# Kernel tuning notes

Hardware: AMD Instinct MI355X
Metric: run time of the kernel (lower is better)

The kernel has to match this reference:

```python
import jax, jax.numpy as jnp
import numpy as np

B, C, L = 4, 256, 4096
C8 = C // 8

def setup_inputs() -> dict:
    key = jax.random.key(0)
    ks = jax.random.split(key, 8)
    s = 1.0 / np.sqrt(C)
    x = jax.random.normal(ks[0], (B, C, L), dtype=jnp.float32)
    Wq = jax.random.normal(ks[1], (C8, C), dtype=jnp.float32) * s
    bq = jax.random.normal(ks[2], (C8,), dtype=jnp.float32) * s
    Wk = jax.random.normal(ks[3], (C8, C), dtype=jnp.float32) * s
    bk = jax.random.normal(ks[4], (C8,), dtype=jnp.float32) * s
    Wv = jax.random.normal(ks[5], (C, C), dtype=jnp.float32) * s
    bv = jax.random.normal(ks[6], (C,), dtype=jnp.float32) * s
    gamma = jax.random.normal(ks[7], (1,), dtype=jnp.float32) * 0.1
    return {"x": x, "Wq": Wq, "bq": bq, "Wk": Wk, "bk": bk, "Wv": Wv, "bv": bv, "gamma": gamma}

def reference(x, Wq, bq, Wk, bk, Wv, bv, gamma):
    # pointwise conv1d == channel matmul: [O,C] x [B,C,L] -> [B,O,L]
    q = jnp.einsum('oc,bcl->bol', Wq, x) + bq[None, :, None]   # [B, C8, L]
    k = jnp.einsum('oc,bcl->bol', Wk, x) + bk[None, :, None]   # [B, C8, L]
    v = jnp.einsum('oc,bcl->bol', Wv, x) + bv[None, :, None]   # [B, C,  L]
    # attention[b,i,j] = sum_c q[b,c,i] * k[b,c,j]
    attn = jnp.einsum('bci,bcj->bij', q, k)                    # [B, L, L]
    attn = jax.nn.softmax(attn, axis=-1)
    # out[b,c,i] = sum_j v[b,c,j] * attn[b,i,j]
    out = jnp.einsum('bcj,bij->bci', v, attn)                  # [B, C, L]
    return gamma * out + x
```

## Files before the change

### kernel.cpp

```cpp
#include <hip/hip_runtime.h>
#include <math.h>

#define BB 4
#define CC 256
#define LL 4096
#define DD 32
#define LOG2E 1.44269504088896f

typedef __attribute__((ext_vector_type(8))) short short8;
typedef __attribute__((ext_vector_type(4))) short short4v;
typedef __attribute__((ext_vector_type(4))) float f32x4;
typedef __attribute__((ext_vector_type(16))) float f32x16;
typedef __attribute__((ext_vector_type(4))) unsigned int uint4v;
typedef __attribute__((ext_vector_type(2))) unsigned int uint2v;

#define BARRIER() asm volatile("s_waitcnt lgkmcnt(0)\n\ts_barrier" ::: "memory")

__device__ inline unsigned short f2bf(float f) {
  union { float f; unsigned u; } v; v.f = f;
  unsigned r = v.u + 0x7fffu + ((v.u >> 16) & 1u);
  return (unsigned short)(r >> 16);
}

__device__ inline float fast_exp2(float x) {
#if __has_builtin(__builtin_amdgcn_exp2f)
  return __builtin_amdgcn_exp2f(x);
#else
  return exp2f(x);
#endif
}

__global__ __launch_bounds__(256) void wprep_kernel(
    const float* __restrict__ Wq, const float* __restrict__ Wk, const float* __restrict__ Wv,
    unsigned short* __restrict__ wf)
{
  const int t = threadIdx.x;
  const int ot = blockIdx.x >> 1;
  const int rep = blockIdx.x & 1;
  const int lane = t & 63, cl = lane & 15, q4 = lane >> 4;
  const int ks = (t >> 6) + 4 * rep;
  const int o = ot * 16 + cl;
  const int c = ks * 32 + q4 * 8;
  const float* src = (o < 32) ? (Wq + o * CC) : (o < 64) ? (Wk + (o - 32) * CC)
                                              : (Wv + (o - 64) * CC);
  const float sc = (o < 32) ? LOG2E : 1.0f;
  unsigned short p[8];
  #pragma unroll
  for (int j = 0; j < 8; ++j) p[j] = f2bf(src[c + j] * sc);
  uint4v u;
  u.x = (unsigned)p[0] | ((unsigned)p[1] << 16);
  u.y = (unsigned)p[2] | ((unsigned)p[3] << 16);
  u.z = (unsigned)p[4] | ((unsigned)p[5] << 16);
  u.w = (unsigned)p[6] | ((unsigned)p[7] << 16);
  *(uint4v*)(wf + ((size_t)(ot * 8 + ks) * 64 + lane) * 8) = u;
}

__global__ __launch_bounds__(512, 4) void qkv_kernel(
    const float* __restrict__ x, const unsigned short* __restrict__ wf,
    const float* __restrict__ bq, const float* __restrict__ bk, const float* __restrict__ bv,
    unsigned short* __restrict__ qF, unsigned short* __restrict__ kF,
    unsigned short* __restrict__ vF)
{
  __shared__ union {
    float xl[32 * 261];
    struct {
      unsigned short qk[32 * 72];
      __align__(16) unsigned short v[256 * 40];
    } ep;
  } sm;

  const int t = threadIdx.x;
  const int lane = t & 63, cl = lane & 15, q4 = lane >> 4;
  const int blk = blockIdx.x;
  const int b  = (blk & 7) >> 1;
  const int it = ((blk >> 3) << 1) + (blk & 1);
  const int i0 = it * 32;

  {
    const int ln8 = t & 7;
    #pragma unroll
    for (int p = 0; p < 4; ++p) {
      const int c = (t >> 3) + 64 * p;
      const f32x4 v = *(const f32x4*)(x + ((size_t)(b * CC + c)) * LL + i0 + ln8 * 4);
      #pragma unroll
      for (int k = 0; k < 4; ++k) sm.xl[(ln8 * 4 + k) * 261 + c] = v[k];
    }
  }
  __syncthreads();

  const int wi = (t >> 6) & 1, wo = t >> 7;
  const f32x4 zero = {0.f, 0.f, 0.f, 0.f};
  f32x4 acc[5];
  #pragma unroll
  for (int u = 0; u < 5; ++u) acc[u] = zero;

  for (int ks = 0; ks < 8; ++ks) {
    unsigned short p[8];
    #pragma unroll
    for (int j = 0; j < 8; ++j)
      p[j] = f2bf(sm.xl[(16 * wi + cl) * 261 + ks * 32 + q4 * 8 + j]);
    union { short8 s; uint4v u; } bfr;
    bfr.u.x = (unsigned)p[0] | ((unsigned)p[1] << 16);
    bfr.u.y = (unsigned)p[2] | ((unsigned)p[3] << 16);
    bfr.u.z = (unsigned)p[4] | ((unsigned)p[5] << 16);
    bfr.u.w = (unsigned)p[6] | ((unsigned)p[7] << 16);
    #pragma unroll
    for (int u = 0; u < 5; ++u) {
      const short8 a = *(const short8*)(wf + ((size_t)((wo * 5 + u) * 8 + ks) * 64 + lane) * 8);
      acc[u] = __builtin_amdgcn_mfma_f32_16x16x32_bf16(a, bfr.s, acc[u], 0, 0, 0);
    }
  }
  __syncthreads();

  #pragma unroll
  for (int u = 0; u < 5; ++u) {
    const int g = wo * 5 + u;
    if (g < 4) {
      short4v pk;
      #pragma unroll
      for (int r = 0; r < 4; ++r) {
        const int o = 16 * g + 4 * q4 + r;
        const float v = acc[u][r] + ((o < 32) ? bq[o] * LOG2E : bk[o - 32]);
        pk[r] = (short)f2bf(v);
      }
      *(short4v*)&sm.ep.qk[(16 * wi + cl) * 72 + 16 * g + 4 * q4] = pk;
    } else {
      #pragma unroll
      for (int r = 0; r < 4; ++r) {
        const int ch = 16 * (g - 4) + 4 * q4 + r;
        sm.ep.v[ch * 40 + 16 * wi + cl] = f2bf(acc[u][r] + bv[ch]);
      }
    }
  }
  __syncthreads();

  if (t < 256) {
    const int which = t >> 7;
    const int c = (t >> 6) & 1;
    const int l = t & 63, hi2 = l >> 5, ql2 = l & 31;
    const uint4v d = *(const uint4v*)&sm.ep.qk[ql2 * 72 + which * 32 + c * 16 + hi2 * 8];
    unsigned short* dstf = which ? kF : qF;
    *(uint4v*)(dstf + (((size_t)(b * 128 + it) * 2 + c) * 64 + l) * 8) = d;
  }
  #pragma unroll
  for (int rep = 0; rep < 2; ++rep) {
    const int slot = t + 512 * rep;
    const int fl = slot >> 6, l = slot & 63;
    const int g = fl >> 3, m = fl & 7;
    const int hi2 = l >> 5, cl2 = l & 31;
    const uint4v d = *(const uint4v*)&sm.ep.v[(32 * m + cl2) * 40 + g * 16 + hi2 * 8];
    *(uint4v*)(vF + (((size_t)(b * 256 + 2 * it + g) * 8 + m) * 64 + l) * 8) = d;
  }
}

__global__ __launch_bounds__(768, 3) void attn_kernel(
    const unsigned short* __restrict__ qF, const unsigned short* __restrict__ kF,
    const unsigned short* __restrict__ vF, const float* __restrict__ x,
    const float* __restrict__ gamma_p, float* __restrict__ out)
{
  __shared__ __align__(16) unsigned short P[2 * 8 * 2 * 2 * 512];
  __shared__ float l_lds[8][2][64];

  const int t = threadIdx.x;
  const int w = t >> 6, lane = t & 63, ql = lane & 31, hi = lane >> 5;
  const int blk = blockIdx.x;
  const int b  = (blk & 7) >> 1;
  const int it = ((blk >> 3) << 1) + (blk & 1);
  const int i0 = it * 64;

  if (w < 8) {
    const int pw = w;
    short8 qB[2][2];
    #pragma unroll
    for (int qt = 0; qt < 2; ++qt)
      #pragma unroll
      for (int c = 0; c < 2; ++c)
        qB[qt][c] = *(const short8*)(qF +
            (((size_t)(b * 128 + it * 2 + qt) * 2 + c) * 64 + lane) * 8);
    short8 kA[2];
    #pragma unroll
    for (int c = 0; c < 2; ++c)
      kA[c] = *(const short8*)(kF + (((size_t)(b * 128 + pw) * 2 + c) * 64 + lane) * 8);
    float l_r[2] = {0.f, 0.f};
    const f32x16 z16 = {0.f,0.f,0.f,0.f,0.f,0.f,0.f,0.f,0.f,0.f,0.f,0.f,0.f,0.f,0.f,0.f};

    auto produce = [&](int ss, int buf) {
      f32x16 S[2];
      __builtin_amdgcn_s_setprio(1);
      #pragma unroll
      for (int qt = 0; qt < 2; ++qt)
        S[qt] = __builtin_amdgcn_mfma_f32_32x32x16_bf16(kA[0], qB[qt][0], z16, 0, 0, 0);
      #pragma unroll
      for (int qt = 0; qt < 2; ++qt)
        S[qt] = __builtin_amdgcn_mfma_f32_32x32x16_bf16(kA[1], qB[qt][1], S[qt], 0, 0, 0);
      __builtin_amdgcn_s_setprio(0);
      const int ntile = ((ss + 1) & 15) * 8 + pw;
      #pragma unroll
      for (int c = 0; c < 2; ++c)
        kA[c] = *(const short8*)(kF + (((size_t)(b * 128 + ntile) * 2 + c) * 64 + lane) * 8);
      #pragma unroll
      for (int qt = 0; qt < 2; ++qt) {
        float ex[16];
        #pragma unroll
        for (int r = 0; r < 16; ++r) ex[r] = fast_exp2(S[qt][r]);
        l_r[qt] += ((((ex[0] + ex[1]) + (ex[2] + ex[3])) + ((ex[4] + ex[5]) + (ex[6] + ex[7])))
                 + (((ex[8] + ex[9]) + (ex[10] + ex[11])) + ((ex[12] + ex[13]) + (ex[14] + ex[15]))));
        #pragma unroll
        for (int c = 0; c < 2; ++c) {
          unsigned w0, w1, w2, w3;
          asm("v_cvt_pk_bf16_f32 %0, %1, %2" : "=v"(w0) : "v"(ex[8 * c + 0]), "v"(ex[8 * c + 1]));
          asm("v_cvt_pk_bf16_f32 %0, %1, %2" : "=v"(w1) : "v"(ex[8 * c + 2]), "v"(ex[8 * c + 3]));
          asm("v_cvt_pk_bf16_f32 %0, %1, %2" : "=v"(w2) : "v"(ex[8 * c + 4]), "v"(ex[8 * c + 5]));
          asm("v_cvt_pk_bf16_f32 %0, %1, %2" : "=v"(w3) : "v"(ex[8 * c + 6]), "v"(ex[8 * c + 7]));
          asm("v_permlane32_swap_b32 %0, %1" : "+v"(w0), "+v"(w2));
          asm("v_permlane32_swap_b32 %0, %1" : "+v"(w1), "+v"(w3));
          uint4v u; u.x = w0; u.y = w1; u.z = w2; u.w = w3;
          *(uint4v*)(&P[(((buf * 8 + pw) * 2 + qt) * 2 + c) * 512 + hi * 256 + ql * 8]) = u;
        }
      }
    };

    produce(0, 0);
    __syncthreads();
    for (int i = 0; i < 16; ++i) {
      if (i < 15) produce(i + 1, (i + 1) & 1);
      BARRIER();
    }
    l_lds[pw][0][lane] = l_r[0];
    l_lds[pw][1][lane] = l_r[1];
    BARRIER();
  } else {
    const int mq = w - 8;
    const unsigned short* vroot = vF + (size_t)b * (256 * 8 * 512) + lane * 8;
    f32x16 O[2][2];
    #pragma unroll
    for (int mi = 0; mi < 2; ++mi)
      #pragma unroll
      for (int qt = 0; qt < 2; ++qt) {
        const f32x16 z16 = {0.f,0.f,0.f,0.f,0.f,0.f,0.f,0.f,0.f,0.f,0.f,0.f,0.f,0.f,0.f,0.f};
        O[mi][qt] = z16;
      }
    short8 vA[4][2];
    #pragma unroll
    for (int s = 0; s < 4; ++s)
      #pragma unroll
      for (int mi = 0; mi < 2; ++mi)
        vA[s][mi] = *(const short8*)(vroot + ((size_t)(s * 8 + 2 * mq + mi)) * 512);
    __syncthreads();

    short8 pb[3][2];
    for (int i = 0; i < 16; ++i) {
      const int buf = i & 1;
      #pragma unroll
      for (int s = 0; s < 2; ++s)
        #pragma unroll
        for (int qt = 0; qt < 2; ++qt)
          pb[s][qt] = *(const short8*)(&P[((((buf * 8 + 0) * 2 + qt) * 2 + s) * 512)
                                          + hi * 256 + ql * 8]);
      #pragma unroll
      for (int s = 0; s < 16; ++s) {
        if (s < 14) {
          const int ns = s + 2, kk = ns >> 1, c = ns & 1;
          #pragma unroll
          for (int qt = 0; qt < 2; ++qt)
            pb[ns % 3][qt] = *(const short8*)(&P[((((buf * 8 + kk) * 2 + qt) * 2 + c) * 512)
                                                 + hi * 256 + ql * 8]);
        }
        __builtin_amdgcn_s_setprio(1);
        #pragma unroll
        for (int mi = 0; mi < 2; ++mi)
          #pragma unroll
          for (int qt = 0; qt < 2; ++qt)
            O[mi][qt] = __builtin_amdgcn_mfma_f32_32x32x16_bf16(vA[s & 3][mi], pb[s % 3][qt],
                                                                O[mi][qt], 0, 0, 0);
        __builtin_amdgcn_s_setprio(0);
        const int kg = (i * 16 + s + 4) & 255;
        #pragma unroll
        for (int mi = 0; mi < 2; ++mi)
          vA[s & 3][mi] = *(const short8*)(vroot + ((size_t)(kg * 8 + 2 * mq + mi)) * 512);
      }
      BARRIER();
    }
    BARRIER();

    const float gam = gamma_p[0];
    float inv_l[2];
    #pragma unroll
    for (int qt = 0; qt < 2; ++qt) {
      float s = 0.f;
      #pragma unroll
      for (int pw = 0; pw < 8; ++pw)
        s += l_lds[pw][qt][ql] + l_lds[pw][qt][ql + 32];
      inv_l[qt] = 1.0f / s;
    }
    #pragma unroll
    for (int mi = 0; mi < 2; ++mi)
      #pragma unroll
      for (int qt = 0; qt < 2; ++qt)
        #pragma unroll
        for (int r = 0; r < 16; ++r) {
          const int ch = 64 * mq + 32 * mi + (r & 3) + 8 * (r >> 2) + 4 * hi;
          const int ii = i0 + 32 * qt + ql;
          const size_t idx = ((size_t)b * CC + ch) * LL + ii;
          out[idx] = gam * O[mi][qt][r] * inv_l[qt] + x[idx];
        }
  }
}

extern "C" void kernel_launch(void* const* d_in, const int* in_sizes, int n_in,
                              void* d_out, int out_size, void* d_ws, size_t ws_size,
                              hipStream_t stream) {
  const float* x     = (const float*)d_in[0];
  const float* Wq    = (const float*)d_in[1];
  const float* bq    = (const float*)d_in[2];
  const float* Wk    = (const float*)d_in[3];
  const float* bk    = (const float*)d_in[4];
  const float* Wv    = (const float*)d_in[5];
  const float* bv    = (const float*)d_in[6];
  const float* gamma = (const float*)d_in[7];
  float* out = (float*)d_out;

  unsigned short* qF = (unsigned short*)d_ws;
  unsigned short* kF = qF + (size_t)BB * LL * DD;
  unsigned short* vF = kF + (size_t)BB * LL * DD;
  unsigned short* wf = (unsigned short*)d_out;

  wprep_kernel<<<40, 256, 0, stream>>>(Wq, Wk, Wv, wf);
  qkv_kernel<<<512, 512, 0, stream>>>(x, wf, bq, bk, bv, qF, kF, vF);
  attn_kernel<<<256, 768, 0, stream>>>(qF, kF, vF, x, gamma, out);
}
```

Measured before the change: 133.6 us.

## Restructure QKV projection with 32x32 MFMA and direct fragment-layout stores

The QKV projection kernel now converts x to bf16 fragments in shared memory once. It uses 32x32x16 MFMAs with one wave per output tile, and writes Q/K/V fragments straight from registers using packed bf16 conversion and permlane swaps. This removes the fp32 transpose in LDS, the per-k-step software bf16 rounding, and the epilogue staging through shared memory. The weight-prep kernel is rewritten to match the new fragment layout, and the attention kernel's packing is factored into a shared macro. The projection is a small part of total time next to attention, so the overall effect is limited.

```diff
diff --git a/kernel.cpp b/kernel.cpp
--- a/kernel.cpp
+++ b/kernel.cpp
@@ -16,12 +16,6 @@
 
 #define BARRIER() asm volatile("s_waitcnt lgkmcnt(0)\n\ts_barrier" ::: "memory")
 
-__device__ inline unsigned short f2bf(float f) {
-  union { float f; unsigned u; } v; v.f = f;
-  unsigned r = v.u + 0x7fffu + ((v.u >> 16) & 1u);
-  return (unsigned short)(r >> 16);
-}
-
 __device__ inline float fast_exp2(float x) {
 #if __has_builtin(__builtin_amdgcn_exp2f)
   return __builtin_amdgcn_exp2f(x);
@@ -30,29 +24,44 @@
 #endif
 }
 
+#define PACK8_STORE(EX0,EX1,EX2,EX3,EX4,EX5,EX6,EX7, DSTPTR)                         \
+  {                                                                                  \
+    unsigned pw0, pw1, pw2, pw3;                                                     \
+    asm("v_cvt_pk_bf16_f32 %0, %1, %2" : "=v"(pw0) : "v"(EX0), "v"(EX1));            \
+    asm("v_cvt_pk_bf16_f32 %0, %1, %2" : "=v"(pw1) : "v"(EX2), "v"(EX3));            \
+    asm("v_cvt_pk_bf16_f32 %0, %1, %2" : "=v"(pw2) : "v"(EX4), "v"(EX5));            \
+    asm("v_cvt_pk_bf16_f32 %0, %1, %2" : "=v"(pw3) : "v"(EX6), "v"(EX7));            \
+    asm("v_permlane32_swap_b32 %0, %1" : "+v"(pw0), "+v"(pw2));                      \
+    asm("v_permlane32_swap_b32 %0, %1" : "+v"(pw1), "+v"(pw3));                      \
+    uint4v pu; pu.x = pw0; pu.y = pw1; pu.z = pw2; pu.w = pw3;                       \
+    *(uint4v*)(DSTPTR) = pu;                                                         \
+  }
+
 __global__ __launch_bounds__(256) void wprep_kernel(
     const float* __restrict__ Wq, const float* __restrict__ Wk, const float* __restrict__ Wv,
     unsigned short* __restrict__ wf)
 {
   const int t = threadIdx.x;
-  const int ot = blockIdx.x >> 1;
-  const int rep = blockIdx.x & 1;
-  const int lane = t & 63, cl = lane & 15, q4 = lane >> 4;
-  const int ks = (t >> 6) + 4 * rep;
-  const int o = ot * 16 + cl;
-  const int c = ks * 32 + q4 * 8;
-  const float* src = (o < 32) ? (Wq + o * CC) : (o < 64) ? (Wk + (o - 32) * CC)
-                                              : (Wv + (o - 64) * CC);
-  const float sc = (o < 32) ? LOG2E : 1.0f;
-  unsigned short p[8];
-  #pragma unroll
-  for (int j = 0; j < 8; ++j) p[j] = f2bf(src[c + j] * sc);
-  uint4v u;
-  u.x = (unsigned)p[0] | ((unsigned)p[1] << 16);
-  u.y = (unsigned)p[2] | ((unsigned)p[3] << 16);
-  u.z = (unsigned)p[4] | ((unsigned)p[5] << 16);
-  u.w = (unsigned)p[6] | ((unsigned)p[7] << 16);
-  *(uint4v*)(wf + ((size_t)(ot * 8 + ks) * 64 + lane) * 8) = u;
+  const int g = blockIdx.x * 4 + (t >> 6);
+  const int lane = t & 63, ql = lane & 31, hi = lane >> 5;
+  const int tile = g >> 4, chunk = g & 15;
+  const int cin = chunk * 16 + hi * 8;
+  const float* src;
+  float sc = 1.0f;
+  if (tile == 0)      { src = Wq + (size_t)ql * CC; sc = LOG2E; }
+  else if (tile == 1) { src = Wk + (size_t)ql * CC; }
+  else                { src = Wv + (size_t)(32 * (tile - 2) + ql) * CC; }
+  const f32x4 a = *(const f32x4*)(src + cin);
+  const f32x4 b2 = *(const f32x4*)(src + cin + 4);
+  unsigned w0, w1, w2, w3;
+  const float f0 = a[0] * sc, f1 = a[1] * sc, f2 = a[2] * sc, f3 = a[3] * sc;
+  const float f4 = b2[0] * sc, f5 = b2[1] * sc, f6 = b2[2] * sc, f7 = b2[3] * sc;
+  asm("v_cvt_pk_bf16_f32 %0, %1, %2" : "=v"(w0) : "v"(f0), "v"(f1));
+  asm("v_cvt_pk_bf16_f32 %0, %1, %2" : "=v"(w1) : "v"(f2), "v"(f3));
+  asm("v_cvt_pk_bf16_f32 %0, %1, %2" : "=v"(w2) : "v"(f4), "v"(f5));
+  asm("v_cvt_pk_bf16_f32 %0, %1, %2" : "=v"(w3) : "v"(f6), "v"(f7));
+  uint4v u; u.x = w0; u.y = w1; u.z = w2; u.w = w3;
+  *(uint4v*)(wf + ((size_t)g * 64 + lane) * 8) = u;
 }
 
 __global__ __launch_bounds__(512, 4) void qkv_kernel(
@@ -61,95 +70,76 @@
     unsigned short* __restrict__ qF, unsigned short* __restrict__ kF,
     unsigned short* __restrict__ vF)
 {
-  __shared__ union {
-    float xl[32 * 261];
-    struct {
-      unsigned short qk[32 * 72];
-      __align__(16) unsigned short v[256 * 40];
-    } ep;
-  } sm;
+  __shared__ __align__(16) unsigned short xb[16 * 64 * 8];
 
   const int t = threadIdx.x;
-  const int lane = t & 63, cl = lane & 15, q4 = lane >> 4;
+  const int w = t >> 6, lane = t & 63, ql = lane & 31, hi = lane >> 5;
   const int blk = blockIdx.x;
   const int b  = (blk & 7) >> 1;
   const int it = ((blk >> 3) << 1) + (blk & 1);
   const int i0 = it * 32;
 
+  #pragma unroll
+  for (int e = 0; e < 2; ++e) {
+    const int cc = 2 * w + e;
+    const float* xs = x + ((size_t)(b * CC + cc * 16 + hi * 8)) * LL + i0 + ql;
+    float f[8];
+    #pragma unroll
+    for (int j = 0; j < 8; ++j) f[j] = xs[(size_t)j * LL];
+    unsigned w0, w1, w2, w3;
+    asm("v_cvt_pk_bf16_f32 %0, %1, %2" : "=v"(w0) : "v"(f[0]), "v"(f[1]));
+    asm("v_cvt_pk_bf16_f32 %0, %1, %2" : "=v"(w1) : "v"(f[2]), "v"(f[3]));
+    asm("v_cvt_pk_bf16_f32 %0, %1, %2" : "=v"(w2) : "v"(f[4]), "v"(f[5]));
+    asm("v_cvt_pk_bf16_f32 %0, %1, %2" : "=v"(w3) : "v"(f[6]), "v"(f[7]));
+    uint4v u; u.x = w0; u.y = w1; u.z = w2; u.w = w3;
+    *(uint4v*)&xb[(cc * 64 + lane) * 8] = u;
+  }
+  __syncthreads();
+
+  const f32x16 z16 = {0.f,0.f,0.f,0.f,0.f,0.f,0.f,0.f,0.f,0.f,0.f,0.f,0.f,0.f,0.f,0.f};
+
   {
-    const int ln8 = t & 7;
-    #pragma unroll
-    for (int p = 0; p < 4; ++p) {
-      const int c = (t >> 3) + 64 * p;
-      const f32x4 v = *(const f32x4*)(x + ((size_t)(b * CC + c)) * LL + i0 + ln8 * 4);
-      #pragma unroll
-      for (int k = 0; k < 4; ++k) sm.xl[(ln8 * 4 + k) * 261 + c] = v[k];
-    }
-  }
-  __syncthreads();
-
-  const int wi = (t >> 6) & 1, wo = t >> 7;
-  const f32x4 zero = {0.f, 0.f, 0.f, 0.f};
-  f32x4 acc[5];
-  #pragma unroll
-  for (int u = 0; u < 5; ++u) acc[u] = zero;
-
-  for (int ks = 0; ks < 8; ++ks) {
-    unsigned short p[8];
-    #pragma unroll
-    for (int j = 0; j < 8; ++j)
-      p[j] = f2bf(sm.xl[(16 * wi + cl) * 261 + ks * 32 + q4 * 8 + j]);
-    union { short8 s; uint4v u; } bfr;
-    bfr.u.x = (unsigned)p[0] | ((unsigned)p[1] << 16);
-    bfr.u.y = (unsigned)p[2] | ((unsigned)p[3] << 16);
-    bfr.u.z = (unsigned)p[4] | ((unsigned)p[5] << 16);
-    bfr.u.w = (unsigned)p[6] | ((unsigned)p[7] << 16);
-    #pragma unroll
-    for (int u = 0; u < 5; ++u) {
-      const short8 a = *(const short8*)(wf + ((size_t)((wo * 5 + u) * 8 + ks) * 64 + lane) * 8);
-      acc[u] = __builtin_amdgcn_mfma_f32_16x16x32_bf16(a, bfr.s, acc[u], 0, 0, 0);
-    }
-  }
-  __syncthreads();
-
-  #pragma unroll
-  for (int u = 0; u < 5; ++u) {
-    const int g = wo * 5 + u;
-    if (g < 4) {
-      short4v pk;
-      #pragma unroll
-      for (int r = 0; r < 4; ++r) {
-        const int o = 16 * g + 4 * q4 + r;
-        const float v = acc[u][r] + ((o < 32) ? bq[o] * LOG2E : bk[o - 32]);
-        pk[r] = (short)f2bf(v);
-      }
-      *(short4v*)&sm.ep.qk[(16 * wi + cl) * 72 + 16 * g + 4 * q4] = pk;
-    } else {
-      #pragma unroll
-      for (int r = 0; r < 4; ++r) {
-        const int ch = 16 * (g - 4) + 4 * q4 + r;
-        sm.ep.v[ch * 40 + 16 * wi + cl] = f2bf(acc[u][r] + bv[ch]);
-      }
-    }
-  }
-  __syncthreads();
-
-  if (t < 256) {
-    const int which = t >> 7;
-    const int c = (t >> 6) & 1;
-    const int l = t & 63, hi2 = l >> 5, ql2 = l & 31;
-    const uint4v d = *(const uint4v*)&sm.ep.qk[ql2 * 72 + which * 32 + c * 16 + hi2 * 8];
-    unsigned short* dstf = which ? kF : qF;
-    *(uint4v*)(dstf + (((size_t)(b * 128 + it) * 2 + c) * 64 + l) * 8) = d;
-  }
-  #pragma unroll
-  for (int rep = 0; rep < 2; ++rep) {
-    const int slot = t + 512 * rep;
-    const int fl = slot >> 6, l = slot & 63;
-    const int g = fl >> 3, m = fl & 7;
-    const int hi2 = l >> 5, cl2 = l & 31;
-    const uint4v d = *(const uint4v*)&sm.ep.v[(32 * m + cl2) * 40 + g * 16 + hi2 * 8];
-    *(uint4v*)(vF + (((size_t)(b * 256 + 2 * it + g) * 8 + m) * 64 + l) * 8) = d;
+    f32x16 D = z16;
+    #pragma unroll
+    for (int c = 0; c < 16; ++c) {
+      const short8 xc = *(const short8*)&xb[(c * 64 + lane) * 8];
+      const short8 wv = *(const short8*)(wf + ((size_t)((2 + w) * 16 + c) * 64 + lane) * 8);
+      D = __builtin_amdgcn_mfma_f32_32x32x16_bf16(xc, wv, D, 0, 0, 0);
+    }
+    const float bvv = bv[32 * w + ql];
+    #pragma unroll
+    for (int r = 0; r < 16; ++r) D[r] += bvv;
+    #pragma unroll
+    for (int s = 0; s < 2; ++s) {
+      unsigned short* dst = vF + (((size_t)(b * 256 + 2 * it + s) * 8 + w) * 64 + lane) * 8;
+      PACK8_STORE(D[8*s+0], D[8*s+1], D[8*s+2], D[8*s+3],
+                  D[8*s+4], D[8*s+5], D[8*s+6], D[8*s+7], dst);
+    }
+  }
+
+  if (w < 2) {
+    const float* bsrc = w ? bk : bq;
+    const float bscale = w ? 1.0f : LOG2E;
+    float br[16];
+    #pragma unroll
+    for (int r = 0; r < 16; ++r)
+      br[r] = bsrc[(r & 3) + 8 * (r >> 2) + 4 * hi] * bscale;
+    f32x16 D = z16;
+    #pragma unroll
+    for (int c = 0; c < 16; ++c) {
+      const short8 xc = *(const short8*)&xb[(c * 64 + lane) * 8];
+      const short8 wa = *(const short8*)(wf + ((size_t)(w * 16 + c) * 64 + lane) * 8);
+      D = __builtin_amdgcn_mfma_f32_32x32x16_bf16(wa, xc, D, 0, 0, 0);
+    }
+    #pragma unroll
+    for (int r = 0; r < 16; ++r) D[r] += br[r];
+    unsigned short* basef = w ? kF : qF;
+    #pragma unroll
+    for (int s = 0; s < 2; ++s) {
+      unsigned short* dst = basef + (((size_t)(b * 128 + it) * 2 + s) * 64 + lane) * 8;
+      PACK8_STORE(D[8*s+0], D[8*s+1], D[8*s+2], D[8*s+3],
+                  D[8*s+4], D[8*s+5], D[8*s+6], D[8*s+7], dst);
+    }
   }
 }
 
@@ -207,15 +197,9 @@
                  + (((ex[8] + ex[9]) + (ex[10] + ex[11])) + ((ex[12] + ex[13]) + (ex[14] + ex[15]))));
         #pragma unroll
         for (int c = 0; c < 2; ++c) {
-          unsigned w0, w1, w2, w3;
-          asm("v_cvt_pk_bf16_f32 %0, %1, %2" : "=v"(w0) : "v"(ex[8 * c + 0]), "v"(ex[8 * c + 1]));
-          asm("v_cvt_pk_bf16_f32 %0, %1, %2" : "=v"(w1) : "v"(ex[8 * c + 2]), "v"(ex[8 * c + 3]));
-          asm("v_cvt_pk_bf16_f32 %0, %1, %2" : "=v"(w2) : "v"(ex[8 * c + 4]), "v"(ex[8 * c + 5]));
-          asm("v_cvt_pk_bf16_f32 %0, %1, %2" : "=v"(w3) : "v"(ex[8 * c + 6]), "v"(ex[8 * c + 7]));
-          asm("v_permlane32_swap_b32 %0, %1" : "+v"(w0), "+v"(w2));
-          asm("v_permlane32_swap_b32 %0, %1" : "+v"(w1), "+v"(w3));
-          uint4v u; u.x = w0; u.y = w1; u.z = w2; u.w = w3;
-          *(uint4v*)(&P[(((buf * 8 + pw) * 2 + qt) * 2 + c) * 512 + hi * 256 + ql * 8]) = u;
+          unsigned short* dst = &P[(((buf * 8 + pw) * 2 + qt) * 2 + c) * 512 + hi * 256 + ql * 8];
+          PACK8_STORE(ex[8*c+0], ex[8*c+1], ex[8*c+2], ex[8*c+3],
+                      ex[8*c+4], ex[8*c+5], ex[8*c+6], ex[8*c+7], dst);
         }
       }
     };
```

After: 129.8 us. 2.8% less time.
